# Performance work log

Hardware: AMD Instinct MI355X
Metric: run time of the kernel (lower is better)

The kernel has to match this reference:

```python
import jax, jax.numpy as jnp
import numpy as np

B, N, P = 8, 4096, 1024
P4 = P // 4
EPS = 1e-5


def _ln(x, g, b):
    mu = jnp.mean(x, axis=-1, keepdims=True)
    var = jnp.var(x, axis=-1, keepdims=True)
    return (x - mu) * jax.lax.rsqrt(var + EPS) * g + b


def setup_inputs() -> dict:
    key = jax.random.key(0)
    ks = jax.random.split(key, 16)
    s = lambda fan: 1.0 / np.sqrt(fan)
    return {
        "xyz": jax.random.normal(ks[0], (B, N, 3), jnp.float32),
        "x": jax.random.normal(ks[1], (B, N, P), jnp.float32),
        "ln1_g": jnp.ones((P,), jnp.float32),
        "ln1_b": jnp.zeros((P,), jnp.float32),
        "ln2_g": jnp.ones((P,), jnp.float32),
        "ln2_b": jnp.zeros((P,), jnp.float32),
        "qk_w": jax.random.normal(ks[2], (P4, P), jnp.float32) * s(P),   # shared q/k 1x1 conv, no bias
        "v_w": jax.random.normal(ks[3], (P, P), jnp.float32) * s(P),
        "v_b": jax.random.normal(ks[4], (P,), jnp.float32) * s(P),
        "t1_w": jax.random.normal(ks[5], (P, P4), jnp.float32) * s(P4),  # trans_conv
        "t1_b": jax.random.normal(ks[6], (P,), jnp.float32) * s(P4),
        "t2_w": jax.random.normal(ks[7], (P, P4), jnp.float32) * s(P4),  # trans_conv1
        "t2_b": jax.random.normal(ks[8], (P,), jnp.float32) * s(P4),
        "m1_w": jax.random.normal(ks[9], (P, P), jnp.float32) * s(P),
        "m1_b": jax.random.normal(ks[10], (P,), jnp.float32) * s(P),
        "m2_w": jax.random.normal(ks[11], (P, P), jnp.float32) * s(P),
        "m2_b": jax.random.normal(ks[12], (P,), jnp.float32) * s(P),
    }


def reference(xyz, x, ln1_g, ln1_b, ln2_g, ln2_b, qk_w, v_w, v_b,
              t1_w, t1_b, t2_w, t2_b, m1_w, m1_b, m2_w, m2_b):
    # xyz is accepted but unused, matching the torch module. Dropout = eval identity.
    res1 = x
    h = _ln(x, ln1_g, ln1_b)                                   # [B,N,P]
    # TransformerBlock_1 (1x1 convs on h^T [B,P,N] are just matmuls over P)
    x_q = jnp.einsum('op,bnp->bon', qk_w, h)                   # [B,P4,N]
    # k shares weights with q; x_k permuted is x_q transposed
    x_v = jnp.einsum('op,bnp->bno', v_w, h) + v_b              # [B,N,P]
    energy = jnp.einsum('bqn,bkn->bqk', x_q, x_q)              # [B,P4,P4]
    att = jnp.einsum('op,bpk->bok', t1_w, energy) + t1_b[:, None]   # [B,P,P4]
    att = jax.nn.gelu(att, approximate=False)
    att = jnp.einsum('op,bkp->bok', t2_w, att) + t2_b[:, None]      # [B,P,P]
    att = jax.nn.softmax(att, axis=-1)
    t_out = jnp.einsum('bnp,bpq->bnq', x_v, att)               # [B,N,P]
    x1 = t_out + res1
    h2 = _ln(x1, ln2_g, ln2_b)
    m = jax.nn.gelu(h2 @ m1_w.T + m1_b, approximate=False)
    m = m @ m2_w.T + m2_b
    return x1 + m
```

## Files before the change

kernel.cpp:

```cpp
#include <hip/hip_runtime.h>


typedef __attribute__((ext_vector_type(4))) float f32x4;
typedef __attribute__((ext_vector_type(8))) _Float16 h16x8;
typedef __attribute__((ext_vector_type(8))) unsigned short u16x8;
typedef __attribute__((ext_vector_type(4))) unsigned short u16x4;

__device__ __forceinline__ unsigned short f2h(float f) {
  _Float16 h = (_Float16)f;
  return __builtin_bit_cast(unsigned short, h);
}
__device__ __forceinline__ unsigned split16(float f) {
  _Float16 h = (_Float16)f;
  _Float16 l = (_Float16)(f - (float)h);
  return (unsigned)__builtin_bit_cast(unsigned short, h) |
         ((unsigned)__builtin_bit_cast(unsigned short, l) << 16);
}
__device__ __forceinline__ float gelu_f(float x) {
  return 0.5f * x * (1.0f + erff(x * 0.70710678118654752f));
}
__device__ __forceinline__ void gload16(const void* g, void* l) {
  __builtin_amdgcn_global_load_lds(
      (const __attribute__((address_space(1))) unsigned int*)g,
      (__attribute__((address_space(3))) unsigned int*)l, 16, 0, 0);
}
#define FENCE() asm volatile("" ::: "memory")

__global__ __launch_bounds__(256)
void ln_kernel(const float* __restrict__ x, const float* __restrict__ g,
               const float* __restrict__ b, unsigned short* __restrict__ hi,
               unsigned short* __restrict__ lo) {
  __shared__ float red[16];
  const size_t base = (size_t)blockIdx.x * 1024;
  const int t = threadIdx.x;
  f32x4 v = *(const f32x4*)&x[base + t * 4];
  float s = v[0] + v[1] + v[2] + v[3];
  float q = v[0] * v[0] + v[1] * v[1] + v[2] * v[2] + v[3] * v[3];
#pragma unroll
  for (int o = 32; o > 0; o >>= 1) { s += __shfl_down(s, o); q += __shfl_down(q, o); }
  const int w = t >> 6;
  if ((t & 63) == 0) { red[w] = s; red[8 + w] = q; }
  __syncthreads();
  s = (red[0] + red[1]) + (red[2] + red[3]);
  q = (red[8] + red[9]) + (red[10] + red[11]);
  const float mu = s * (1.0f / 1024.0f);
  const float var = q * (1.0f / 1024.0f) - mu * mu;
  const float is = rsqrtf(var + 1e-5f);
  f32x4 gg = *(const f32x4*)&g[t * 4];
  f32x4 bb = *(const f32x4*)&b[t * 4];
  u16x4 oh, ol;
#pragma unroll
  for (int j = 0; j < 4; j++) {
    float y = (v[j] - mu) * is * gg[j] + bb[j];
    unsigned p = split16(y);
    oh[j] = (unsigned short)(p & 0xffffu);
    ol[j] = (unsigned short)(p >> 16);
  }
  *(u16x4*)&hi[base + t * 4] = oh;
  if (lo) *(u16x4*)&lo[base + t * 4] = ol;
}

__global__ __launch_bounds__(256)
void cvt_kernel(const float* __restrict__ in, unsigned short* __restrict__ hi,
                unsigned short* __restrict__ lo, int n4) {
  int i = blockIdx.x * 256 + threadIdx.x;
  if (i < n4) {
    f32x4 v = *(const f32x4*)&in[(size_t)i * 4];
    u16x4 oh, ol;
#pragma unroll
    for (int j = 0; j < 4; j++) {
      unsigned p = split16(v[j]);
      oh[j] = (unsigned short)(p & 0xffffu);
      ol[j] = (unsigned short)(p >> 16);
    }
    *(u16x4*)&hi[(size_t)i * 4] = oh;
    if (lo) *(u16x4*)&lo[(size_t)i * 4] = ol;
  }
}

template <int EPI>
__global__ __launch_bounds__(512)
void gemm_v(const unsigned short* __restrict__ Ain, const unsigned short* __restrict__ Bin,
            void* __restrict__ Cout, const float* __restrict__ bias,
            const float* __restrict__ resIn,
            int K, int lda, int ldb, int ldc,
            long long sA, long long sB, long long sC, long long sRes) {
  __shared__ short As[2][16384];
  __shared__ short Bs[2][16384];
  const int z = blockIdx.z;
  const unsigned short* A = Ain + (size_t)z * sA;
  const unsigned short* B = Bin + (size_t)z * sB;
  int bx = blockIdx.x, by = blockIdx.y;
  {
    const int nwg = gridDim.x * gridDim.y;
    if ((nwg & 7) == 0 && nwg >= 16) {
      const int flat = bx + gridDim.x * by;
      const int chunk = nwg >> 3;
      const int nf = (flat & 7) * chunk + (flat >> 3);
      bx = nf % gridDim.x;
      by = nf / gridDim.x;
    }
  }
  const int mBase = by * 256, nBase = bx * 256;
  const int t = threadIdx.x, w = t >> 6, l = t & 63;
  const int r16 = l & 15, kq = l >> 4;
  const int wr = (w >> 2) * 128, wc = (w & 3) * 64;
  f32x4 acc[8][4] = {};

  auto stage = [&](int buf, int k0) {
#pragma unroll
    for (int i = 0; i < 4; ++i) {
      const int c = i * 512 + t;
      const int row = c >> 3, cc = c & 7;
      const int gc = cc ^ (row & 7);
      const int cbase = i * 512 + w * 64;
      gload16(&A[(size_t)(mBase + row) * lda + k0 + gc * 8], &As[buf][cbase * 8]);
      gload16(&B[(size_t)(nBase + row) * ldb + k0 + gc * 8], &Bs[buf][cbase * 8]);
    }
  };

  const int nt = K >> 6;
  stage(0, 0);
  if (nt > 1) stage(1, 64);
  for (int ts = 0; ts < nt; ++ts) {
    const int cur = ts & 1;
    if (ts + 1 < nt) { asm volatile("s_waitcnt vmcnt(8)" ::: "memory"); }
    else             { asm volatile("s_waitcnt vmcnt(0)" ::: "memory"); }
    __builtin_amdgcn_s_barrier();
    FENCE();
#pragma unroll
    for (int kk = 0; kk < 2; ++kk) {
      h16x8 aF[8], bF[4];
#pragma unroll
      for (int ni = 0; ni < 4; ni++) {
        const int r = wc + ni * 16 + r16;
        bF[ni] = *(const h16x8*)&Bs[cur][r * 64 + (((kk * 4 + kq) ^ (r & 7))) * 8];
      }
#pragma unroll
      for (int mi = 0; mi < 8; mi++) {
        const int r = wr + mi * 16 + r16;
        aF[mi] = *(const h16x8*)&As[cur][r * 64 + (((kk * 4 + kq) ^ (r & 7))) * 8];
      }
#pragma unroll
      for (int mi = 0; mi < 8; mi++)
#pragma unroll
        for (int ni = 0; ni < 4; ni++)
          acc[mi][ni] = __builtin_amdgcn_mfma_f32_16x16x32_f16(aF[mi], bF[ni], acc[mi][ni], 0, 0, 0);
    }
    FENCE();
    __builtin_amdgcn_s_barrier();
    FENCE();
    if (ts + 2 < nt) stage(cur, (ts + 2) * 64);
  }

  unsigned short* C16 = (unsigned short*)Cout + (size_t)z * sC;
  float* C32 = (float*)Cout + (size_t)z * sC;
  const float* res = (EPI >= 2) ? (resIn + (size_t)z * sRes) : nullptr;
#pragma unroll
  for (int mi = 0; mi < 8; mi++) {
#pragma unroll
    for (int ni = 0; ni < 4; ni++) {
      const int cl = nBase + wc + ni * 16 + r16;
      const float bcol = (EPI != 2) ? bias[cl] : 0.0f;
#pragma unroll
      for (int r = 0; r < 4; r++) {
        const int rw = mBase + wr + mi * 16 + kq * 4 + r;
        float v = acc[mi][ni][r] + bcol;
        if (EPI == 1) v = gelu_f(v);
        if (EPI >= 2) v += res[(size_t)rw * ldc + cl];
        if (EPI <= 1) C16[(size_t)rw * ldc + cl] = f2h(v);
        else          C32[(size_t)rw * ldc + cl] = v;
      }
    }
  }
}

template <int EPI>
__global__ __launch_bounds__(256)
void gemm_s(const unsigned short* __restrict__ Ahi, const unsigned short* __restrict__ Alo,
            const unsigned short* __restrict__ Bhi, const unsigned short* __restrict__ Blo,
            void* __restrict__ Cout, unsigned short* __restrict__ Cout2,
            const float* __restrict__ bias,
            int K, int lda, int ldb, int ldc,
            long long sA, long long sB, long long sC, int splitK) {
  __shared__ short As[2][8192];
  __shared__ short Bs[2][8192];
  const int z = blockIdx.z;
  const int bi = z / splitK, sp = z % splitK;
  const int kLen = K / splitK, kStart = sp * kLen;
  const unsigned short* AH = Ahi + (size_t)bi * sA;
  const unsigned short* BH = Bhi + (size_t)bi * sB;
  const unsigned short* AL = Alo + (size_t)bi * sA;
  const unsigned short* BL = Blo + (size_t)bi * sB;
  int bx = blockIdx.x, by = blockIdx.y;
  {
    const int nwg = gridDim.x * gridDim.y;
    if ((nwg & 7) == 0 && nwg >= 16) {
      const int flat = bx + gridDim.x * by;
      const int chunk = nwg >> 3;
      const int nf = (flat & 7) * chunk + (flat >> 3);
      bx = nf % gridDim.x;
      by = nf / gridDim.x;
    }
  }
  const int mBase = by * 128, nBase = bx * 128;
  const int t = threadIdx.x, w = t >> 6, l = t & 63;
  const int r16 = l & 15, kq = l >> 4;
  const int wr = (w >> 1) * 64, wc = (w & 1) * 64;
  f32x4 acc[4][4] = {};

  auto stage = [&](int buf, int k0) {
#pragma unroll
    for (int i = 0; i < 2; ++i) {
      const int c = i * 256 + t;
      const int row = c >> 2, cc = c & 3;
      const int gc = cc ^ ((row >> 1) & 3);
      const int cbase = i * 256 + w * 64;
      const size_t ga = (size_t)(mBase + row) * lda + k0 + gc * 8;
      const size_t gb = (size_t)(nBase + row) * ldb + k0 + gc * 8;
      gload16(&AH[ga], &As[buf][cbase * 8]);
      gload16(&AL[ga], &As[buf][4096 + cbase * 8]);
      gload16(&BH[gb], &Bs[buf][cbase * 8]);
      gload16(&BL[gb], &Bs[buf][4096 + cbase * 8]);
    }
  };

  const int nsteps = kLen >> 5;
  stage(0, kStart);
  if (nsteps > 1) stage(1, kStart + 32);
  for (int ts = 0; ts < nsteps; ++ts) {
    const int cur = ts & 1;
    if (ts + 1 < nsteps) { asm volatile("s_waitcnt vmcnt(8)" ::: "memory"); }
    else                 { asm volatile("s_waitcnt vmcnt(0)" ::: "memory"); }
    __builtin_amdgcn_s_barrier();
    FENCE();
    h16x8 aH[4], bH[4], aL[4], bL[4];
#pragma unroll
    for (int mi = 0; mi < 4; mi++) {
      const int r = wr + mi * 16 + r16;
      const int off = r * 32 + (kq ^ ((r >> 1) & 3)) * 8;
      aH[mi] = *(const h16x8*)&As[cur][off];
      aL[mi] = *(const h16x8*)&As[cur][4096 + off];
    }
#pragma unroll
    for (int ni = 0; ni < 4; ni++) {
      const int r = wc + ni * 16 + r16;
      const int off = r * 32 + (kq ^ ((r >> 1) & 3)) * 8;
      bH[ni] = *(const h16x8*)&Bs[cur][off];
      bL[ni] = *(const h16x8*)&Bs[cur][4096 + off];
    }
#pragma unroll
    for (int mi = 0; mi < 4; mi++)
#pragma unroll
      for (int ni = 0; ni < 4; ni++) {
        acc[mi][ni] = __builtin_amdgcn_mfma_f32_16x16x32_f16(aH[mi], bH[ni], acc[mi][ni], 0, 0, 0);
        acc[mi][ni] = __builtin_amdgcn_mfma_f32_16x16x32_f16(aH[mi], bL[ni], acc[mi][ni], 0, 0, 0);
        acc[mi][ni] = __builtin_amdgcn_mfma_f32_16x16x32_f16(aL[mi], bH[ni], acc[mi][ni], 0, 0, 0);
      }
    FENCE();
    __builtin_amdgcn_s_barrier();
    FENCE();
    if (ts + 2 < nsteps) stage(cur, kStart + (ts + 2) * 32);
  }

  unsigned short* C16 = (unsigned short*)Cout + (size_t)z * sC;
  unsigned short* C16b = Cout2 ? Cout2 + (size_t)z * sC : nullptr;
  float* C32 = (float*)Cout + (size_t)z * sC;
#pragma unroll
  for (int mi = 0; mi < 4; mi++) {
#pragma unroll
    for (int ni = 0; ni < 4; ni++) {
      const int cl = nBase + wc + ni * 16 + r16;
#pragma unroll
      for (int r = 0; r < 4; r++) {
        const int rw = mBase + wr + mi * 16 + kq * 4 + r;
        float v = acc[mi][ni][r];
        if (EPI == 6 || EPI == 7) v += bias[rw];
        if (EPI == 6) v = gelu_f(v);
        const size_t idx = (size_t)rw * ldc + cl;
        if (EPI == 4 || EPI == 6) {
          unsigned p = split16(v);
          C16[idx] = (unsigned short)(p & 0xffffu);
          C16b[idx] = (unsigned short)(p >> 16);
        } else {
          C32[idx] = v;
        }
      }
    }
  }
}

__global__ __launch_bounds__(256)
void ereduce_kernel(const float* __restrict__ part, unsigned short* __restrict__ ehi,
                    unsigned short* __restrict__ elo) {
  const size_t idx = (size_t)blockIdx.x * 256 + threadIdx.x;
  const size_t b = idx >> 16, i = idx & 65535;
  const float* p = part + b * (8ull * 65536) + i;
  float s0 = (p[0] + p[65536]) + (p[2 * 65536] + p[3 * 65536]);
  float s1 = (p[4 * 65536] + p[5 * 65536]) + (p[6 * 65536] + p[7 * 65536]);
  unsigned pk = split16(s0 + s1);
  ehi[idx] = (unsigned short)(pk & 0xffffu);
  elo[idx] = (unsigned short)(pk >> 16);
}

__global__ __launch_bounds__(256)
void smax_t_kernel(const float* __restrict__ a2, unsigned short* __restrict__ attT) {
  __shared__ float S[8][1028];
  __shared__ float inv[8];
  const int t = threadIdx.x;
  const int b = blockIdx.y;
  const int o0 = blockIdx.x * 8;
  const float* src = a2 + ((size_t)b * 1024 + o0) * 1024;
#pragma unroll
  for (int i = 0; i < 8; i++)
    *(f32x4*)&S[i][t * 4] = *(const f32x4*)&src[(size_t)i * 1024 + t * 4];
  __syncthreads();
  const int w = t >> 6, l = t & 63;
  for (int rr = 0; rr < 2; rr++) {
    const int r = w * 2 + rr;
    float m = -1e30f;
#pragma unroll
    for (int i = 0; i < 16; i++) m = fmaxf(m, S[r][l + i * 64]);
#pragma unroll
    for (int o = 32; o > 0; o >>= 1) m = fmaxf(m, __shfl_xor(m, o));
    float ssum = 0.0f;
#pragma unroll
    for (int i = 0; i < 16; i++) {
      float e = expf(S[r][l + i * 64] - m);
      S[r][l + i * 64] = e;
      ssum += e;
    }
#pragma unroll
    for (int o = 32; o > 0; o >>= 1) ssum += __shfl_xor(ssum, o);
    if (l == 0) inv[r] = 1.0f / ssum;
  }
  __syncthreads();
  float iv[8];
#pragma unroll
  for (int r = 0; r < 8; r++) iv[r] = inv[r];
#pragma unroll
  for (int i = 0; i < 4; i++) {
    const int k = i * 256 + t;
    u16x8 ov;
#pragma unroll
    for (int r = 0; r < 8; r++) ov[r] = f2h(S[r][k] * iv[r]);
    *(u16x8*)&attT[((size_t)b * 1024 + k) * 1024 + o0] = ov;
  }
}

extern "C" void kernel_launch(void* const* d_in, const int* in_sizes, int n_in,
                              void* d_out, int out_size, void* d_ws, size_t ws_size,
                              hipStream_t stream) {
  (void)in_sizes; (void)n_in; (void)out_size; (void)ws_size;
  const float* x     = (const float*)d_in[1];
  const float* ln1_g = (const float*)d_in[2];
  const float* ln1_b = (const float*)d_in[3];
  const float* ln2_g = (const float*)d_in[4];
  const float* ln2_b = (const float*)d_in[5];
  const float* qk_w  = (const float*)d_in[6];
  const float* v_w   = (const float*)d_in[7];
  const float* v_b   = (const float*)d_in[8];
  const float* t1_w  = (const float*)d_in[9];
  const float* t1_b  = (const float*)d_in[10];
  const float* t2_w  = (const float*)d_in[11];
  const float* t2_b  = (const float*)d_in[12];
  const float* m1_w  = (const float*)d_in[13];
  const float* m1_b  = (const float*)d_in[14];
  const float* m2_w  = (const float*)d_in[15];
  const float* m2_b  = (const float*)d_in[16];

  char* ws = (char*)d_ws;
  unsigned short* hhi  = (unsigned short*)(ws + 0);
  unsigned short* hlo  = (unsigned short*)(ws + 67108864);
  unsigned short* Qthi = (unsigned short*)(ws + 134217728);
  unsigned short* Qtlo = (unsigned short*)(ws + 150994944);
  float*          part = (float*)(ws + 167772160);
  unsigned short* Ehi  = (unsigned short*)(ws + 184549376);
  unsigned short* Elo  = (unsigned short*)(ws + 185597952);
  unsigned short* Ghi  = (unsigned short*)(ws + 186646528);
  unsigned short* Glo  = (unsigned short*)(ws + 190840832);
  float*          a2   = (float*)(ws + 195035136);
  unsigned short* attT = (unsigned short*)(ws + 228589568);
  unsigned short* xv   = (unsigned short*)(ws + 245366784);
  float*          x1   = (float*)(ws + 312475648);
  unsigned short* wqh  = (unsigned short*)(ws + 446693376);
  unsigned short* wql  = (unsigned short*)(ws + 447217664);
  unsigned short* wv   = (unsigned short*)(ws + 447741952);
  unsigned short* wt1h = (unsigned short*)(ws + 449839104);
  unsigned short* wt1l = (unsigned short*)(ws + 450363392);
  unsigned short* wt2h = (unsigned short*)(ws + 450887680);
  unsigned short* wt2l = (unsigned short*)(ws + 451411968);
  unsigned short* wm1  = (unsigned short*)(ws + 451936256);
  unsigned short* wm2  = (unsigned short*)(ws + 454033408);
  unsigned short* h2 = hhi;
  unsigned short* gb = hlo;
  float* out = (float*)d_out;

  cvt_kernel<<<dim3(256),  dim3(256), 0, stream>>>(qk_w, wqh, wql, 65536);
  cvt_kernel<<<dim3(1024), dim3(256), 0, stream>>>(v_w, wv, nullptr, 262144);
  cvt_kernel<<<dim3(256),  dim3(256), 0, stream>>>(t1_w, wt1h, wt1l, 65536);
  cvt_kernel<<<dim3(256),  dim3(256), 0, stream>>>(t2_w, wt2h, wt2l, 65536);
  cvt_kernel<<<dim3(1024), dim3(256), 0, stream>>>(m1_w, wm1, nullptr, 262144);
  cvt_kernel<<<dim3(1024), dim3(256), 0, stream>>>(m2_w, wm2, nullptr, 262144);
  ln_kernel<<<dim3(32768), dim3(256), 0, stream>>>(x, ln1_g, ln1_b, hhi, hlo);
  gemm_s<4><<<dim3(32, 2, 8), dim3(256), 0, stream>>>(
      wqh, wql, hhi, hlo, Qthi, Qtlo, nullptr,
      1024, 1024, 1024, 4096, 0, 4194304, 1048576, 1);
  gemm_v<0><<<dim3(4, 128, 1), dim3(512), 0, stream>>>(
      hhi, wv, xv, v_b, nullptr, 1024, 1024, 1024, 1024, 0, 0, 0, 0);
  gemm_s<5><<<dim3(2, 2, 64), dim3(256), 0, stream>>>(
      Qthi, Qtlo, Qthi, Qtlo, part, nullptr, nullptr,
      4096, 4096, 4096, 256, 1048576, 1048576, 65536, 8);
  ereduce_kernel<<<dim3(2048), dim3(256), 0, stream>>>(part, Ehi, Elo);
  gemm_s<6><<<dim3(2, 8, 8), dim3(256), 0, stream>>>(
      wt1h, wt1l, Ehi, Elo, Ghi, Glo, t1_b,
      256, 256, 256, 256, 0, 65536, 262144, 1);
  gemm_s<7><<<dim3(8, 8, 8), dim3(256), 0, stream>>>(
      wt2h, wt2l, Ghi, Glo, a2, nullptr, t2_b,
      256, 256, 256, 1024, 0, 262144, 1048576, 1);
  smax_t_kernel<<<dim3(128, 8), dim3(256), 0, stream>>>(a2, attT);
  gemm_v<2><<<dim3(4, 16, 8), dim3(512), 0, stream>>>(
      xv, attT, x1, nullptr, x, 1024, 1024, 1024, 1024, 4194304, 1048576, 4194304, 4194304);
  ln_kernel<<<dim3(32768), dim3(256), 0, stream>>>(x1, ln2_g, ln2_b, h2, nullptr);
  gemm_v<1><<<dim3(4, 128, 1), dim3(512), 0, stream>>>(
      h2, wm1, gb, m1_b, nullptr, 1024, 1024, 1024, 1024, 0, 0, 0, 0);
  gemm_v<3><<<dim3(4, 128, 1), dim3(512), 0, stream>>>(
      gb, wm2, out, m2_b, x1, 1024, 1024, 1024, 1024, 0, 0, 0, 0);
}
```

Measured before the change: 720.7 us.

## Deepen GEMM pipeline to 4 stages, stage epilogue through LDS, add setprio

The main fp16 GEMM kernel now uses a 4-buffer ring of 32-wide K tiles with three tiles in flight instead of double-buffered 64-wide tiles. The aim is to hide more global-load latency behind MFMA work. The fp16-output epilogue is now staged through LDS so each wave writes 16-byte vectorized rows rather than scattered 2-byte stores. s_setprio is raised around the MFMA sections of both GEMM kernels. In exchange there are more barriers per unit of K work, the per-tile swizzle is narrower, and the pipeline assumes K is at least 96.

```diff
diff --git a/kernel.cpp b/kernel.cpp
--- a/kernel.cpp
+++ b/kernel.cpp
@@ -79,14 +79,15 @@
 }
 
 template <int EPI>
-__global__ __launch_bounds__(512)
+__global__ __launch_bounds__(512, 1)
 void gemm_v(const unsigned short* __restrict__ Ain, const unsigned short* __restrict__ Bin,
             void* __restrict__ Cout, const float* __restrict__ bias,
             const float* __restrict__ resIn,
             int K, int lda, int ldb, int ldc,
             long long sA, long long sB, long long sC, long long sRes) {
-  __shared__ short As[2][16384];
-  __shared__ short Bs[2][16384];
+  __shared__ short LDSall[65536];
+  short* LA = LDSall;
+  short* LB = LDSall + 32768;
   const int z = blockIdx.z;
   const unsigned short* A = Ain + (size_t)z * sA;
   const unsigned short* B = Bin + (size_t)z * sB;
@@ -109,37 +110,39 @@
 
   auto stage = [&](int buf, int k0) {
 #pragma unroll
-    for (int i = 0; i < 4; ++i) {
+    for (int i = 0; i < 2; ++i) {
       const int c = i * 512 + t;
-      const int row = c >> 3, cc = c & 7;
-      const int gc = cc ^ (row & 7);
-      const int cbase = i * 512 + w * 64;
-      gload16(&A[(size_t)(mBase + row) * lda + k0 + gc * 8], &As[buf][cbase * 8]);
-      gload16(&B[(size_t)(nBase + row) * ldb + k0 + gc * 8], &Bs[buf][cbase * 8]);
+      const int row = c >> 2, cc = c & 3;
+      const int gc = cc ^ ((row >> 1) & 3);
+      const int cb = i * 512 + w * 64;
+      gload16(&A[(size_t)(mBase + row) * lda + k0 + gc * 8], &LA[buf * 8192 + cb * 8]);
+      gload16(&B[(size_t)(nBase + row) * ldb + k0 + gc * 8], &LB[buf * 8192 + cb * 8]);
     }
   };
 
-  const int nt = K >> 6;
+  const int nt = K >> 5;
   stage(0, 0);
-  if (nt > 1) stage(1, 64);
+  stage(1, 32);
+  stage(2, 64);
   for (int ts = 0; ts < nt; ++ts) {
-    const int cur = ts & 1;
-    if (ts + 1 < nt) { asm volatile("s_waitcnt vmcnt(8)" ::: "memory"); }
-    else             { asm volatile("s_waitcnt vmcnt(0)" ::: "memory"); }
+    const int buf = ts & 3;
+    if (ts + 3 <= nt) { asm volatile("s_waitcnt vmcnt(8)" ::: "memory"); }
+    else if (ts + 2 == nt) { asm volatile("s_waitcnt vmcnt(4)" ::: "memory"); }
+    else { asm volatile("s_waitcnt vmcnt(0)" ::: "memory"); }
     __builtin_amdgcn_s_barrier();
     FENCE();
-#pragma unroll
-    for (int kk = 0; kk < 2; ++kk) {
+    __builtin_amdgcn_s_setprio(1);
+    {
       h16x8 aF[8], bF[4];
 #pragma unroll
       for (int ni = 0; ni < 4; ni++) {
         const int r = wc + ni * 16 + r16;
-        bF[ni] = *(const h16x8*)&Bs[cur][r * 64 + (((kk * 4 + kq) ^ (r & 7))) * 8];
+        bF[ni] = *(const h16x8*)&LB[buf * 8192 + r * 32 + ((kq ^ ((r >> 1) & 3))) * 8];
       }
 #pragma unroll
       for (int mi = 0; mi < 8; mi++) {
         const int r = wr + mi * 16 + r16;
-        aF[mi] = *(const h16x8*)&As[cur][r * 64 + (((kk * 4 + kq) ^ (r & 7))) * 8];
+        aF[mi] = *(const h16x8*)&LA[buf * 8192 + r * 32 + ((kq ^ ((r >> 1) & 3))) * 8];
       }
 #pragma unroll
       for (int mi = 0; mi < 8; mi++)
@@ -147,29 +150,53 @@
         for (int ni = 0; ni < 4; ni++)
           acc[mi][ni] = __builtin_amdgcn_mfma_f32_16x16x32_f16(aF[mi], bF[ni], acc[mi][ni], 0, 0, 0);
     }
+    __builtin_amdgcn_s_setprio(0);
     FENCE();
     __builtin_amdgcn_s_barrier();
     FENCE();
-    if (ts + 2 < nt) stage(cur, (ts + 2) * 64);
+    if (ts + 3 < nt) stage((ts + 3) & 3, (ts + 3) * 32);
   }
 
   unsigned short* C16 = (unsigned short*)Cout + (size_t)z * sC;
   float* C32 = (float*)Cout + (size_t)z * sC;
   const float* res = (EPI >= 2) ? (resIn + (size_t)z * sRes) : nullptr;
-#pragma unroll
-  for (int mi = 0; mi < 8; mi++) {
-#pragma unroll
-    for (int ni = 0; ni < 4; ni++) {
-      const int cl = nBase + wc + ni * 16 + r16;
-      const float bcol = (EPI != 2) ? bias[cl] : 0.0f;
-#pragma unroll
-      for (int r = 0; r < 4; r++) {
-        const int rw = mBase + wr + mi * 16 + kq * 4 + r;
-        float v = acc[mi][ni][r] + bcol;
-        if (EPI == 1) v = gelu_f(v);
-        if (EPI >= 2) v += res[(size_t)rw * ldc + cl];
-        if (EPI <= 1) C16[(size_t)rw * ldc + cl] = f2h(v);
-        else          C32[(size_t)rw * ldc + cl] = v;
+
+  if constexpr (EPI <= 1) {
+    short* ep = LDSall + w * 8192;
+#pragma unroll
+    for (int mi = 0; mi < 8; mi++) {
+#pragma unroll
+      for (int ni = 0; ni < 4; ni++) {
+        const int cl = nBase + wc + ni * 16 + r16;
+        const float bcol = bias[cl];
+#pragma unroll
+        for (int r = 0; r < 4; r++) {
+          float v = acc[mi][ni][r] + bcol;
+          if (EPI == 1) v = gelu_f(v);
+          ep[(mi * 16 + kq * 4 + r) * 64 + ni * 16 + r16] = (short)f2h(v);
+        }
+      }
+    }
+#pragma unroll
+    for (int j = 0; j < 16; j++) {
+      const int f = j * 512 + l * 8;
+      const int row = f >> 6, col = f & 63;
+      u16x8 v8 = *(const u16x8*)&ep[f];
+      *(u16x8*)&C16[(size_t)(mBase + wr + row) * ldc + nBase + wc + col] = v8;
+    }
+  } else {
+#pragma unroll
+    for (int mi = 0; mi < 8; mi++) {
+#pragma unroll
+      for (int ni = 0; ni < 4; ni++) {
+        const int cl = nBase + wc + ni * 16 + r16;
+        const float bcol = (EPI == 3) ? bias[cl] : 0.0f;
+#pragma unroll
+        for (int r = 0; r < 4; r++) {
+          const int rw = mBase + wr + mi * 16 + kq * 4 + r;
+          float v = acc[mi][ni][r] + bcol + res[(size_t)rw * ldc + cl];
+          C32[(size_t)rw * ldc + cl] = v;
+        }
       }
     }
   }
@@ -249,6 +276,7 @@
       bH[ni] = *(const h16x8*)&Bs[cur][off];
       bL[ni] = *(const h16x8*)&Bs[cur][4096 + off];
     }
+    __builtin_amdgcn_s_setprio(1);
 #pragma unroll
     for (int mi = 0; mi < 4; mi++)
 #pragma unroll
@@ -257,6 +285,7 @@
         acc[mi][ni] = __builtin_amdgcn_mfma_f32_16x16x32_f16(aH[mi], bL[ni], acc[mi][ni], 0, 0, 0);
         acc[mi][ni] = __builtin_amdgcn_mfma_f32_16x16x32_f16(aL[mi], bH[ni], acc[mi][ni], 0, 0, 0);
       }
+    __builtin_amdgcn_s_setprio(0);
     FENCE();
     __builtin_amdgcn_s_barrier();
     FENCE();
```

Measured after the change: 712.9 us. No clear change (-1.1%).
